# Kernel tuning notes

Hardware: AMD Instinct MI355X
Metric: run time of the kernel (lower is better)

Reference implementation:

```python
import jax, jax.numpy as jnp
import numpy as np

RATE, KEEP_K = 4, 1
TAU, ALPHA = 0.1, 0.7
LN_EPS = 1e-5


def setup_inputs() -> dict:
    key = jax.random.key(0)
    k1, k2, k3 = jax.random.split(key, 3)
    B, D, T = 16, 1024, 4096
    x = jax.random.normal(k1, (B, D, T), dtype=jnp.float32)
    W_proj = jax.random.normal(k2, (D, D), dtype=jnp.float32) * 0.02
    b_proj = jnp.zeros((D,), dtype=jnp.float32)
    ln_g = jnp.ones((D,), dtype=jnp.float32)
    ln_b = jnp.zeros((D,), dtype=jnp.float32)
    w_score = jax.random.normal(k3, (D,), dtype=jnp.float32) * 0.02
    return {"x": x, "W_proj": W_proj, "b_proj": b_proj,
            "ln_g": ln_g, "ln_b": ln_b, "w_score": w_score}


def reference(x, W_proj, b_proj, ln_g, ln_b, w_score):
    # x: [B, D, T]; chunks of width w=RATE along T (T divisible by RATE)
    B, D, T = x.shape
    C, w, k = T // RATE, RATE, KEEP_K
    r = w - k
    tokens = x.reshape(B, D, C, w).transpose(0, 2, 3, 1)          # [B,C,w,D]

    # metric_proj (torch Linear: y = x W^T + b), computed once and reused
    feat = jnp.einsum('bcwd,ed->bcwe', tokens, W_proj) + b_proj   # [B,C,w,D]

    # F.normalize(feat, dim=-1) with eps=1e-12
    nrm = jnp.maximum(jnp.linalg.norm(feat, axis=-1, keepdims=True), 1e-12)
    metric = feat / nrm
    sim = jnp.einsum('bcwd,bcvd->bcwv', metric, metric)           # [B,C,w,w]
    sim = jnp.where(jnp.eye(w, dtype=bool), 0.0, sim)

    # score head: LayerNorm(feat) @ w_score (no bias)
    mu = feat.mean(-1, keepdims=True)
    var = ((feat - mu) ** 2).mean(-1, keepdims=True)
    s_pred = jnp.einsum('bcwd,d->bcw',
                        ((feat - mu) / jnp.sqrt(var + LN_EPS)) * ln_g + ln_b,
                        w_score)                                   # [B,C,w]

    imp_norm = jnp.linalg.norm(tokens, axis=-1)                    # [B,C,w]
    s_mix = ALPHA * s_pred + (1.0 - ALPHA) * imp_norm
    attn = jax.nn.softmax(sim / TAU, axis=-1)                      # [B,C,w,w]

    # top-k kept tokens per chunk (descending, matches torch.topk)
    _, top_idx = jax.lax.top_k(s_mix, k)                           # [B,C,k]
    kept = jnp.take_along_axis(tokens, top_idx[..., None], axis=2) # [B,C,k,D]

    # rest indices: complement of top_idx in ascending order (matches nonzero)
    pos = jnp.arange(w)
    is_top = (pos[None, None, :, None] == top_idx[:, :, None, :]).any(-1)  # [B,C,w]
    keys = jnp.where(is_top, w, pos)
    rest_idx = jnp.argsort(keys, axis=-1)[..., :r]                 # [B,C,r]

    rest_tokens = jnp.take_along_axis(tokens, rest_idx[..., None], axis=2)  # [B,C,r,D]
    attn_rest = jnp.take_along_axis(attn, rest_idx[..., None], axis=2)      # [B,C,r,w]
    rest_imp = jnp.take_along_axis(attn_rest, top_idx[:, :, None, :], axis=3)  # [B,C,r,k]
    norm_w = rest_imp / (rest_imp.sum(-1, keepdims=True) + 1e-6)
    merged_add = jnp.einsum('bcrk,bcrd->bckd', norm_w, rest_tokens)  # [B,C,k,D]
    kept = kept + merged_add / 2.0

    out = kept.reshape(B, C * k, D).transpose(0, 2, 1)             # [B,D,C*k]
    return out
```

## Files before the change

### kernel.cpp

```cpp
#include <hip/hip_runtime.h>
#include <hip/hip_bf16.h>
#include <math.h>
#include <stdint.h>

#define D_DIM 1024
#define T_DIM 4096
#define B_DIM 16
#define C_DIM 1024
#define NCHUNK (B_DIM * C_DIM)
#define NKT 32
#define TPAIR (T_DIM/2)
#define EPAIR (D_DIM/2)
#define TAU_INV 10.0f
#define ALPHA 0.7f
#define LN_EPS 1e-5f
#define XSCALE 4.0f
#define WSCALE 32.0f
#define INV_SCALE (1.0f/128.0f)

typedef _Float16 h8 __attribute__((ext_vector_type(8)));
typedef float f4 __attribute__((ext_vector_type(4)));

static __device__ __forceinline__ void gload16(const void* g, void* s) {
    __builtin_amdgcn_global_load_lds(
        (const __attribute__((address_space(1))) unsigned int*)g,
        (__attribute__((address_space(3))) unsigned int*)s, 16, 0, 0);
}

__global__ __launch_bounds__(256)
void split_x_kernel(const float* __restrict__ x, uint4* __restrict__ Xh,
                    uint4* __restrict__ Xl)
{
    const int tid = threadIdx.x;
    const int t1 = blockIdx.x * 256;
    const int kt = blockIdx.y;
    const int b  = blockIdx.z;
    const int d0 = kt * 32;
    __shared__ __align__(16) float xs[32][264];
    const float* X = x + ((size_t)b * D_DIM + d0) * T_DIM + t1;
    #pragma unroll
    for (int i = 0; i < 8; i++) {
        int idx = tid + i * 256;
        int d = idx >> 6, tq = idx & 63;
        *(float4*)&xs[d][tq * 4] = *(const float4*)(X + (size_t)d * T_DIM + tq * 4);
    }
    __syncthreads();
    const size_t rowbase = (size_t)(b * NKT + kt) * TPAIR + (t1 >> 1);
    #pragma unroll
    for (int ch = 0; ch < 4; ch++) {
        int tp_l = ch * 32 + (tid >> 3);
        int sg = tid & 7;
        int pg = sg ^ (tp_l & 7);
        int p = pg >> 2, g = pg & 3;
        int tl = tp_l * 2 + p;
        unsigned hb[8], lb[8];
        #pragma unroll
        for (int j = 0; j < 8; j++) {
            float v = xs[g * 8 + j][tl] * XSCALE;
            _Float16 hv = (_Float16)v;
            float hf = (float)hv;
            _Float16 lv = (_Float16)(v - hf);
            hb[j] = (unsigned)__builtin_bit_cast(unsigned short, hv);
            lb[j] = (unsigned)__builtin_bit_cast(unsigned short, lv);
        }
        uint4 uh, ul;
        uh.x = hb[0] | (hb[1] << 16); uh.y = hb[2] | (hb[3] << 16);
        uh.z = hb[4] | (hb[5] << 16); uh.w = hb[6] | (hb[7] << 16);
        ul.x = lb[0] | (lb[1] << 16); ul.y = lb[2] | (lb[3] << 16);
        ul.z = lb[4] | (lb[5] << 16); ul.w = lb[6] | (lb[7] << 16);
        size_t si = (rowbase + tp_l) * 8 + sg;
        Xh[si] = uh; Xl[si] = ul;
    }
}

__global__ __launch_bounds__(256)
void split_w_kernel(const float* __restrict__ W, uint4* __restrict__ Wh,
                    uint4* __restrict__ Wl)
{
    const int tid = threadIdx.x;
    const int e1 = blockIdx.x * 256;
    const int kt = blockIdx.y;
    const int d0 = kt * 32;
    const size_t rowbase = (size_t)kt * EPAIR + (e1 >> 1);
    #pragma unroll
    for (int ch = 0; ch < 4; ch++) {
        int ep_l = ch * 32 + (tid >> 3);
        int sg = tid & 7;
        int pg = sg ^ (ep_l & 7);
        int p = pg >> 2, g = pg & 3;
        int e = e1 + ep_l * 2 + p;
        const float* src = W + (size_t)e * D_DIM + d0 + g * 8;
        float4 a = *(const float4*)src;
        float4 c = *(const float4*)(src + 4);
        float vv[8] = {a.x, a.y, a.z, a.w, c.x, c.y, c.z, c.w};
        unsigned hb[8], lb[8];
        #pragma unroll
        for (int j = 0; j < 8; j++) {
            float v = vv[j] * WSCALE;
            _Float16 hv = (_Float16)v;
            float hf = (float)hv;
            _Float16 lv = (_Float16)(v - hf);
            hb[j] = (unsigned)__builtin_bit_cast(unsigned short, hv);
            lb[j] = (unsigned)__builtin_bit_cast(unsigned short, lv);
        }
        uint4 uh, ul;
        uh.x = hb[0] | (hb[1] << 16); uh.y = hb[2] | (hb[3] << 16);
        uh.z = hb[4] | (hb[5] << 16); uh.w = hb[6] | (hb[7] << 16);
        ul.x = lb[0] | (lb[1] << 16); ul.y = lb[2] | (lb[3] << 16);
        ul.z = lb[4] | (lb[5] << 16); ul.w = lb[6] | (lb[7] << 16);
        size_t si = (rowbase + ep_l) * 8 + sg;
        Wh[si] = uh; Wl[si] = ul;
    }
}

__global__ __launch_bounds__(256, 2)
void gemm_mfma_kernel(const uint4* __restrict__ Xh, const uint4* __restrict__ Xl,
                      const uint4* __restrict__ Wh, const uint4* __restrict__ Wl,
                      const float* __restrict__ b_proj, const float* __restrict__ ln_g,
                      const float* __restrict__ w_score, float* __restrict__ scal)
{
    const int tid = threadIdx.x;
    const int l   = tid & 63;
    const int wid = tid >> 6;
    const int wm  = wid >> 1, we = wid & 1;

    int sid = blockIdx.x;
    int xcd = sid & 7, jj = sid >> 3;
    int panel = xcd * 64 + (jj >> 3);
    int eblk  = jj & 7;
    int b = panel >> 5, tblk = panel & 31;
    const int t0 = tblk * 128, e0 = eblk * 128;

    __shared__ __align__(16) char lds[32768];
    char* sXh = lds;
    char* sXl = lds + 8192;
    char* sWh = lds + 16384;
    char* sWl = lds + 24576;

    const int h    = (l & 15) >> 1;
    const int slot = (((l & 1) << 2) | (l >> 4)) ^ h;
    const int aoff = (wm * 32 + h) * 128 + slot * 16;
    const int boff = (we * 32 + h) * 128 + slot * 16;

    f4 acc[4][4];
    #pragma unroll
    for (int mi = 0; mi < 4; mi++)
        #pragma unroll
        for (int ni = 0; ni < 4; ni++) acc[mi][ni] = (f4){0.f, 0.f, 0.f, 0.f};

    const char* gXh0 = (const char*)Xh + ((size_t)b * NKT * TPAIR + (size_t)(t0 >> 1)) * 128;
    const char* gXl0 = (const char*)Xl + ((size_t)b * NKT * TPAIR + (size_t)(t0 >> 1)) * 128;
    const char* gWh0 = (const char*)Wh + (size_t)(e0 >> 1) * 128;
    const char* gWl0 = (const char*)Wl + (size_t)(e0 >> 1) * 128;

    const int stg = wid * 2048;
    const int lo16 = l * 16;

    for (int kt = 0; kt < NKT; kt++) {
        const char* pxh = gXh0 + (size_t)kt * (TPAIR * 128);
        const char* pxl = gXl0 + (size_t)kt * (TPAIR * 128);
        const char* pwh = gWh0 + (size_t)kt * (EPAIR * 128);
        const char* pwl = gWl0 + (size_t)kt * (EPAIR * 128);
        gload16(pxh + stg + lo16,        sXh + stg);
        gload16(pxh + stg + 1024 + lo16, sXh + stg + 1024);
        gload16(pxl + stg + lo16,        sXl + stg);
        gload16(pxl + stg + 1024 + lo16, sXl + stg + 1024);
        gload16(pwh + stg + lo16,        sWh + stg);
        gload16(pwh + stg + 1024 + lo16, sWh + stg + 1024);
        gload16(pwl + stg + lo16,        sWl + stg);
        gload16(pwl + stg + 1024 + lo16, sWl + stg + 1024);
        __syncthreads();

        h8 ah[4], al[4], bh[4], bl[4];
        #pragma unroll
        for (int mi = 0; mi < 4; mi++) {
            ah[mi] = *(const h8*)(sXh + aoff + mi * 1024);
            al[mi] = *(const h8*)(sXl + aoff + mi * 1024);
        }
        #pragma unroll
        for (int ni = 0; ni < 4; ni++) {
            bh[ni] = *(const h8*)(sWh + boff + ni * 1024);
            bl[ni] = *(const h8*)(sWl + boff + ni * 1024);
        }
        #pragma unroll
        for (int mi = 0; mi < 4; mi++)
            #pragma unroll
            for (int ni = 0; ni < 4; ni++) {
                acc[mi][ni] = __builtin_amdgcn_mfma_f32_16x16x32_f16(ah[mi], bh[ni], acc[mi][ni], 0, 0, 0);
                acc[mi][ni] = __builtin_amdgcn_mfma_f32_16x16x32_f16(ah[mi], bl[ni], acc[mi][ni], 0, 0, 0);
                acc[mi][ni] = __builtin_amdgcn_mfma_f32_16x16x32_f16(al[mi], bh[ni], acc[mi][ni], 0, 0, 0);
            }
        __syncthreads();
    }

    const int ecol = l & 15;
    float bias[4], q1[4];
    #pragma unroll
    for (int ni = 0; ni < 4; ni++) {
        int e = e0 + we * 64 + ni * 16 + ecol;
        bias[ni] = b_proj[e];
        q1[ni]   = ln_g[e] * w_score[e];
    }
    #pragma unroll
    for (int mi = 0; mi < 4; mi++) {
        float f[4][4];
        #pragma unroll
        for (int ni = 0; ni < 4; ni++)
            #pragma unroll
            for (int r = 0; r < 4; r++)
                f[r][ni] = acc[mi][ni][r] * INV_SCALE + bias[ni];
        float red[18];
        int pi = 0;
        #pragma unroll
        for (int a2 = 0; a2 < 4; a2++)
            #pragma unroll
            for (int b2 = a2; b2 < 4; b2++) {
                float s = 0.f;
                #pragma unroll
                for (int ni = 0; ni < 4; ni++) s = fmaf(f[a2][ni], f[b2][ni], s);
                red[pi++] = s;
            }
        #pragma unroll
        for (int a2 = 0; a2 < 4; a2++) {
            float s1 = 0.f, s2 = 0.f;
            #pragma unroll
            for (int ni = 0; ni < 4; ni++) {
                s1 = fmaf(f[a2][ni], q1[ni], s1);
                s2 += f[a2][ni];
            }
            red[10 + a2] = s1;
            red[14 + a2] = s2;
        }
        #pragma unroll
        for (int v = 0; v < 18; v++) {
            float s = red[v];
            s += __shfl_xor(s, 1);
            s += __shfl_xor(s, 2);
            s += __shfl_xor(s, 4);
            s += __shfl_xor(s, 8);
            red[v] = s;
        }
        if ((l & 15) == 0) {
            int chunk = b * C_DIM + (t0 >> 2) + wm * 16 + mi * 4 + (l >> 4);
            float* dst = scal + (size_t)chunk * 18;
            #pragma unroll
            for (int v = 0; v < 18; v++) atomicAdd(dst + v, red[v]);
        }
    }
}

__global__ __launch_bounds__(256, 2)
void gemm_reduce_kernel(const float* __restrict__ x, const float* __restrict__ W,
                        const float* __restrict__ b_proj, const float* __restrict__ ln_g,
                        const float* __restrict__ w_score, float* __restrict__ scal)
{
    const int tid = threadIdx.x;
    const int tx  = tid & 15;
    const int ty  = tid >> 4;
    const int t0  = blockIdx.x * 128;
    const int e0  = blockIdx.y * 128;
    const int b   = blockIdx.z;
    const float* X = x + (size_t)b * D_DIM * T_DIM;

    __shared__ __align__(16) float Xs[32][128];
    __shared__ __align__(16) float Ws[32][132];

    float acc[8][8];
    #pragma unroll
    for (int i = 0; i < 8; i++)
        #pragma unroll
        for (int j = 0; j < 8; j++) acc[i][j] = 0.f;

    for (int k0 = 0; k0 < D_DIM; k0 += 32) {
        #pragma unroll
        for (int i = 0; i < 4; i++) {
            int idx = tid + i * 256;
            int dr = idx >> 5, cl = idx & 31;
            const float4 v = *(const float4*)(X + (size_t)(k0 + dr) * T_DIM + t0 + cl * 4);
            *(float4*)&Xs[dr][cl * 4] = v;
        }
        #pragma unroll
        for (int i = 0; i < 4; i++) {
            int idx = tid + i * 256;
            int er = idx >> 3, ck = idx & 7;
            const float4 v = *(const float4*)(W + (size_t)(e0 + er) * D_DIM + k0 + ck * 4);
            Ws[ck * 4 + 0][er] = v.x;
            Ws[ck * 4 + 1][er] = v.y;
            Ws[ck * 4 + 2][er] = v.z;
            Ws[ck * 4 + 3][er] = v.w;
        }
        __syncthreads();
        #pragma unroll 8
        for (int k = 0; k < 32; k++) {
            const float4 xa = *(const float4*)&Xs[k][ty * 8];
            const float4 xb = *(const float4*)&Xs[k][ty * 8 + 4];
            const float4 wa = *(const float4*)&Ws[k][tx * 4];
            const float4 wb = *(const float4*)&Ws[k][64 + tx * 4];
            const float xm[8] = {xa.x, xa.y, xa.z, xa.w, xb.x, xb.y, xb.z, xb.w};
            const float wn[8] = {wa.x, wa.y, wa.z, wa.w, wb.x, wb.y, wb.z, wb.w};
            #pragma unroll
            for (int i = 0; i < 8; i++)
                #pragma unroll
                for (int j = 0; j < 8; j++)
                    acc[i][j] = fmaf(xm[i], wn[j], acc[i][j]);
        }
        __syncthreads();
    }

    float bv[8], q1v[8];
    #pragma unroll
    for (int j = 0; j < 8; j++) {
        int n = (j < 4) ? (tx * 4 + j) : (64 + tx * 4 + (j - 4));
        int e = e0 + n;
        bv[j]  = b_proj[e];
        q1v[j] = ln_g[e] * w_score[e];
    }
    #pragma unroll
    for (int i = 0; i < 8; i++)
        #pragma unroll
        for (int j = 0; j < 8; j++) acc[i][j] += bv[j];

    #pragma unroll
    for (int hh = 0; hh < 2; hh++) {
        float red[18];
        int p = 0;
        #pragma unroll
        for (int a = 0; a < 4; a++)
            #pragma unroll
            for (int b2 = a; b2 < 4; b2++) {
                float s = 0.f;
                #pragma unroll
                for (int j = 0; j < 8; j++) s = fmaf(acc[hh * 4 + a][j], acc[hh * 4 + b2][j], s);
                red[p++] = s;
            }
        #pragma unroll
        for (int a = 0; a < 4; a++) {
            float s1 = 0.f, s2 = 0.f;
            #pragma unroll
            for (int j = 0; j < 8; j++) {
                s1 = fmaf(acc[hh * 4 + a][j], q1v[j], s1);
                s2 += acc[hh * 4 + a][j];
            }
            red[10 + a] = s1;
            red[14 + a] = s2;
        }
        #pragma unroll
        for (int v = 0; v < 18; v++) {
            float s = red[v];
            s += __shfl_xor(s, 1);
            s += __shfl_xor(s, 2);
            s += __shfl_xor(s, 4);
            s += __shfl_xor(s, 8);
            red[v] = s;
        }
        if (tx == 0) {
            int chunk = b * C_DIM + (t0 >> 2) + ty * 2 + hh;
            float* dst = scal + (size_t)chunk * 18;
            #pragma unroll
            for (int v = 0; v < 18; v++) atomicAdd(dst + v, red[v]);
        }
    }
}

__global__ __launch_bounds__(256, 4)
void toknorm_kernel(const float* __restrict__ x, float* __restrict__ tokN2)
{
    const int tt = threadIdx.x & 63;
    const int ds = threadIdx.x >> 6;
    const int t  = blockIdx.x * 64 + tt;
    const int b  = blockIdx.y;
    const float* X = x + (size_t)b * D_DIM * T_DIM + t;
    float s = 0.f;
    const int d0 = ds * 256;
    for (int d = d0; d < d0 + 256; d++) {
        float v = X[(size_t)d * T_DIM];
        s = fmaf(v, v, s);
    }
    __shared__ float lred[256];
    lred[threadIdx.x] = s;
    __syncthreads();
    if (ds == 0)
        tokN2[b * T_DIM + t] = lred[tt] + lred[64 + tt] + lred[128 + tt] + lred[192 + tt];
}

__global__ __launch_bounds__(256, 4)
void coef_kernel(const float* __restrict__ scal, const float* __restrict__ tokN2,
                 const float* __restrict__ ln_g, const float* __restrict__ ln_b,
                 const float* __restrict__ w_score, float* __restrict__ coef)
{
    const int tid = threadIdx.x;
    float p1 = 0.f, p2 = 0.f;
    for (int d = tid; d < D_DIM; d += 256) {
        float wsv = w_score[d];
        p1 = fmaf(ln_g[d], wsv, p1);
        p2 = fmaf(ln_b[d], wsv, p2);
    }
    __shared__ float r1[256], r2[256];
    r1[tid] = p1; r2[tid] = p2;
    __syncthreads();
    for (int s = 128; s > 0; s >>= 1) {
        if (tid < s) { r1[tid] += r1[tid + s]; r2[tid] += r2[tid + s]; }
        __syncthreads();
    }
    const float c1 = r1[0], c2 = r2[0];

    const int chunk = blockIdx.x * 256 + tid;
    const float* s = scal + (size_t)chunk * 18;
    float G[4][4];
    G[0][0] = s[0]; G[0][1] = s[1]; G[0][2] = s[2]; G[0][3] = s[3];
    G[1][1] = s[4]; G[1][2] = s[5]; G[1][3] = s[6];
    G[2][2] = s[7]; G[2][3] = s[8]; G[3][3] = s[9];
    G[1][0] = G[0][1]; G[2][0] = G[0][2]; G[3][0] = G[0][3];
    G[2][1] = G[1][2]; G[3][1] = G[1][3]; G[3][2] = G[2][3];

    const int b = chunk >> 10;
    const int c = chunk & 1023;

    float smix[4], nrm[4];
    #pragma unroll
    for (int i = 0; i < 4; i++) {
        float mu  = s[14 + i] * (1.f / 1024.f);
        float var = G[i][i] * (1.f / 1024.f) - mu * mu;
        float sig = sqrtf(var + LN_EPS);
        float spred = (s[10 + i] - mu * c1) / sig + c2;
        float imp = sqrtf(tokN2[b * T_DIM + c * 4 + i]);
        smix[i] = ALPHA * spred + (1.f - ALPHA) * imp;
        nrm[i]  = fmaxf(sqrtf(G[i][i]), 1e-12f);
    }
    int top = 0; float best = smix[0];
    #pragma unroll
    for (int i = 1; i < 4; i++)
        if (smix[i] > best) { best = smix[i]; top = i; }

    float sim[4][4];
    #pragma unroll
    for (int i = 0; i < 4; i++)
        #pragma unroll
        for (int j = 0; j < 4; j++)
            sim[i][j] = (i == j) ? 0.f : G[i][j] / (nrm[i] * nrm[j]);

    float cf[4];
    #pragma unroll
    for (int r = 0; r < 4; r++) {
        if (r == top) { cf[r] = 1.f; continue; }
        float z[4], m = -1e30f;
        #pragma unroll
        for (int j = 0; j < 4; j++) { z[j] = sim[r][j] * TAU_INV; m = fmaxf(m, z[j]); }
        float denom = 0.f, num = 0.f;
        #pragma unroll
        for (int j = 0; j < 4; j++) {
            float e = expf(z[j] - m);
            denom += e;
            if (j == top) num = e;
        }
        float a = num / denom;
        cf[r] = 0.5f * (a / (a + 1e-6f));
    }
    *(float4*)(coef + (size_t)chunk * 4) = make_float4(cf[0], cf[1], cf[2], cf[3]);
}

__global__ __launch_bounds__(256, 8)
void out_kernel(const float* __restrict__ x, const float* __restrict__ coef,
                float* __restrict__ out)
{
    const size_t gid = (size_t)blockIdx.x * 256 + threadIdx.x;
    const int    c   = (int)(gid & 1023);
    const size_t bd  = gid >> 10;
    const int    b   = (int)(bd >> 10);
    const float4 xv = *(const float4*)(x + (bd << 12) + (size_t)c * 4);
    const float4 cf = *(const float4*)(coef + ((size_t)(b << 10) + c) * 4);
    out[gid] = xv.x * cf.x + xv.y * cf.y + xv.z * cf.z + xv.w * cf.w;
}

extern "C" void kernel_launch(void* const* d_in, const int* in_sizes, int n_in,
                              void* d_out, int out_size, void* d_ws, size_t ws_size,
                              hipStream_t stream)
{
    const float* x   = (const float*)d_in[0];
    const float* W   = (const float*)d_in[1];
    const float* bp  = (const float*)d_in[2];
    const float* g   = (const float*)d_in[3];
    const float* lb  = (const float*)d_in[4];
    const float* wsc = (const float*)d_in[5];
    float* out = (float*)d_out;

    const size_t XH_BYTES = (size_t)B_DIM * NKT * TPAIR * 128;
    const size_t WH_BYTES = (size_t)NKT * EPAIR * 128;
    const size_t NEED = 2 * XH_BYTES + 2 * WH_BYTES
                      + (size_t)NCHUNK * 18 * 4 + (size_t)B_DIM * T_DIM * 4
                      + (size_t)NCHUNK * 4 * 4;

    if (ws_size >= NEED) {
        char* w0 = (char*)d_ws;
        uint4* Xh = (uint4*)w0;
        uint4* Xl = (uint4*)(w0 + XH_BYTES);
        uint4* Wh = (uint4*)(w0 + 2 * XH_BYTES);
        uint4* Wl = (uint4*)(w0 + 2 * XH_BYTES + WH_BYTES);
        float* scal  = (float*)(w0 + 2 * XH_BYTES + 2 * WH_BYTES);
        float* tokN2 = scal + (size_t)NCHUNK * 18;
        float* coef  = tokN2 + (size_t)B_DIM * T_DIM;

        hipMemsetAsync(scal, 0, (size_t)NCHUNK * 18 * sizeof(float), stream);
        split_x_kernel<<<dim3(T_DIM / 256, NKT, B_DIM), 256, 0, stream>>>(x, Xh, Xl);
        split_w_kernel<<<dim3(D_DIM / 256, NKT), 256, 0, stream>>>(W, Wh, Wl);
        toknorm_kernel<<<dim3(T_DIM / 64, B_DIM), 256, 0, stream>>>(x, tokN2);
        gemm_mfma_kernel<<<4096, 256, 0, stream>>>(Xh, Xl, Wh, Wl, bp, g, wsc, scal);
        coef_kernel<<<NCHUNK / 256, 256, 0, stream>>>(scal, tokN2, g, lb, wsc, coef);
        out_kernel<<<(B_DIM * D_DIM * C_DIM) / 256, 256, 0, stream>>>(x, coef, out);
    } else {
        float* scal  = (float*)d_ws;
        float* tokN2 = scal + (size_t)NCHUNK * 18;
        float* coef  = tokN2 + (size_t)B_DIM * T_DIM;

        hipMemsetAsync(scal, 0, (size_t)NCHUNK * 18 * sizeof(float), stream);
        dim3 gA(T_DIM / 128, D_DIM / 128, B_DIM);
        gemm_reduce_kernel<<<gA, 256, 0, stream>>>(x, W, bp, g, wsc, scal);
        toknorm_kernel<<<dim3(T_DIM / 64, B_DIM), 256, 0, stream>>>(x, tokN2);
        coef_kernel<<<NCHUNK / 256, 256, 0, stream>>>(scal, tokN2, g, lb, wsc, coef);
        out_kernel<<<(B_DIM * D_DIM * C_DIM) / 256, 256, 0, stream>>>(x, coef, out);
    }
}
```

Before: 1.326 ms.

## Double-buffer GEMM LDS tiles and fuse token-norm into split_x

The MFMA GEMM main loop now uses two 32KB LDS buffers: it prefetches the next k-tile via global_load_lds while computing on the current one, which halves the barriers per iteration and hides load latency. The token squared-norm computation is folded into split_x_kernel using atomicAdd per token, removing the separate toknorm kernel and its extra full read of x. The cost is doubled LDS (64KB), which may limit occupancy against the 2-blocks-per-CU launch bound, plus atomic traffic on tokN2.

```diff
diff --git a/kernel.cpp b/kernel.cpp
--- a/kernel.cpp
+++ b/kernel.cpp
@@ -29,7 +29,7 @@
 
 __global__ __launch_bounds__(256)
 void split_x_kernel(const float* __restrict__ x, uint4* __restrict__ Xh,
-                    uint4* __restrict__ Xl)
+                    uint4* __restrict__ Xl, float* __restrict__ tokN2)
 {
     const int tid = threadIdx.x;
     const int t1 = blockIdx.x * 256;
@@ -54,9 +54,12 @@
         int p = pg >> 2, g = pg & 3;
         int tl = tp_l * 2 + p;
         unsigned hb[8], lb[8];
+        float n2 = 0.f;
         #pragma unroll
         for (int j = 0; j < 8; j++) {
-            float v = xs[g * 8 + j][tl] * XSCALE;
+            float raw = xs[g * 8 + j][tl];
+            n2 = fmaf(raw, raw, n2);
+            float v = raw * XSCALE;
             _Float16 hv = (_Float16)v;
             float hf = (float)hv;
             _Float16 lv = (_Float16)(v - hf);
@@ -70,6 +73,7 @@
         ul.z = lb[4] | (lb[5] << 16); ul.w = lb[6] | (lb[7] << 16);
         size_t si = (rowbase + tp_l) * 8 + sg;
         Xh[si] = uh; Xl[si] = ul;
+        atomicAdd(&tokN2[b * T_DIM + t1 + tl], n2);
     }
 }
 
@@ -131,11 +135,7 @@
     int b = panel >> 5, tblk = panel & 31;
     const int t0 = tblk * 128, e0 = eblk * 128;
 
-    __shared__ __align__(16) char lds[32768];
-    char* sXh = lds;
-    char* sXl = lds + 8192;
-    char* sWh = lds + 16384;
-    char* sWl = lds + 24576;
+    __shared__ __align__(16) char lds[65536];
 
     const int h    = (l & 15) >> 1;
     const int slot = (((l & 1) << 2) | (l >> 4)) ^ h;
@@ -156,31 +156,33 @@
     const int stg = wid * 2048;
     const int lo16 = l * 16;
 
-    for (int kt = 0; kt < NKT; kt++) {
+    auto stage = [&](int off, int kt) {
         const char* pxh = gXh0 + (size_t)kt * (TPAIR * 128);
         const char* pxl = gXl0 + (size_t)kt * (TPAIR * 128);
         const char* pwh = gWh0 + (size_t)kt * (EPAIR * 128);
         const char* pwl = gWl0 + (size_t)kt * (EPAIR * 128);
-        gload16(pxh + stg + lo16,        sXh + stg);
-        gload16(pxh + stg + 1024 + lo16, sXh + stg + 1024);
-        gload16(pxl + stg + lo16,        sXl + stg);
-        gload16(pxl + stg + 1024 + lo16, sXl + stg + 1024);
-        gload16(pwh + stg + lo16,        sWh + stg);
-        gload16(pwh + stg + 1024 + lo16, sWh + stg + 1024);
-        gload16(pwl + stg + lo16,        sWl + stg);
-        gload16(pwl + stg + 1024 + lo16, sWl + stg + 1024);
-        __syncthreads();
-
+        char* base = lds + off;
+        gload16(pxh + stg + lo16,        base + stg);
+        gload16(pxh + stg + 1024 + lo16, base + stg + 1024);
+        gload16(pxl + stg + lo16,        base + 8192 + stg);
+        gload16(pxl + stg + 1024 + lo16, base + 8192 + stg + 1024);
+        gload16(pwh + stg + lo16,        base + 16384 + stg);
+        gload16(pwh + stg + 1024 + lo16, base + 16384 + stg + 1024);
+        gload16(pwl + stg + lo16,        base + 24576 + stg);
+        gload16(pwl + stg + 1024 + lo16, base + 24576 + stg + 1024);
+    };
+    auto compute = [&](int off) {
+        const char* base = lds + off;
         h8 ah[4], al[4], bh[4], bl[4];
         #pragma unroll
         for (int mi = 0; mi < 4; mi++) {
-            ah[mi] = *(const h8*)(sXh + aoff + mi * 1024);
-            al[mi] = *(const h8*)(sXl + aoff + mi * 1024);
+            ah[mi] = *(const h8*)(base + aoff + mi * 1024);
+            al[mi] = *(const h8*)(base + 8192 + aoff + mi * 1024);
         }
         #pragma unroll
         for (int ni = 0; ni < 4; ni++) {
-            bh[ni] = *(const h8*)(sWh + boff + ni * 1024);
-            bl[ni] = *(const h8*)(sWl + boff + ni * 1024);
+            bh[ni] = *(const h8*)(base + 16384 + boff + ni * 1024);
+            bl[ni] = *(const h8*)(base + 24576 + boff + ni * 1024);
         }
         #pragma unroll
         for (int mi = 0; mi < 4; mi++)
@@ -190,8 +192,22 @@
                 acc[mi][ni] = __builtin_amdgcn_mfma_f32_16x16x32_f16(ah[mi], bl[ni], acc[mi][ni], 0, 0, 0);
                 acc[mi][ni] = __builtin_amdgcn_mfma_f32_16x16x32_f16(al[mi], bh[ni], acc[mi][ni], 0, 0, 0);
             }
-        __syncthreads();
-    }
+    };
+
+    stage(0, 0);
+    asm volatile("s_waitcnt vmcnt(0)" ::: "memory");
+    __builtin_amdgcn_s_barrier();
+
+    int off = 0;
+    #pragma unroll 1
+    for (int kt = 0; kt < NKT - 1; kt++) {
+        stage(off ^ 32768, kt + 1);
+        compute(off);
+        asm volatile("s_waitcnt vmcnt(0)" ::: "memory");
+        __builtin_amdgcn_s_barrier();
+        off ^= 32768;
+    }
+    compute(off);
 
     const int ecol = l & 15;
     float bias[4], q1[4];
@@ -500,10 +516,11 @@
         float* tokN2 = scal + (size_t)NCHUNK * 18;
         float* coef  = tokN2 + (size_t)B_DIM * T_DIM;
 
-        hipMemsetAsync(scal, 0, (size_t)NCHUNK * 18 * sizeof(float), stream);
-        split_x_kernel<<<dim3(T_DIM / 256, NKT, B_DIM), 256, 0, stream>>>(x, Xh, Xl);
+        hipMemsetAsync(scal, 0,
+                       ((size_t)NCHUNK * 18 + (size_t)B_DIM * T_DIM) * sizeof(float),
+                       stream);
+        split_x_kernel<<<dim3(T_DIM / 256, NKT, B_DIM), 256, 0, stream>>>(x, Xh, Xl, tokN2);
         split_w_kernel<<<dim3(D_DIM / 256, NKT), 256, 0, stream>>>(W, Wh, Wl);
-        toknorm_kernel<<<dim3(T_DIM / 64, B_DIM), 256, 0, stream>>>(x, tokN2);
         gemm_mfma_kernel<<<4096, 256, 0, stream>>>(Xh, Xl, Wh, Wl, bp, g, wsc, scal);
         coef_kernel<<<NCHUNK / 256, 256, 0, stream>>>(scal, tokN2, g, lb, wsc, coef);
         out_kernel<<<(B_DIM * D_DIM * C_DIM) / 256, 256, 0, stream>>>(x, coef, out);
```

New measurement: 1.781 ms. 1.34x slower.

## Enlarge MFMA GEMM tile to 256x256 with double-buffered LDS pipeline

Applied to the files above, without the earlier changes.

The split-fp16 GEMM now uses 512-thread blocks computing 256x256 tiles (8x4 accumulators per wave) with a 128KB double-buffered LDS. Global-to-LDS loads for the next k-step are issued in four phases interleaved with MFMA work, using explicit waitcnt, barriers and setprio in place of the previous load-sync-compute-sync loop. The aim is to raise data reuse per loaded byte and hide global load latency behind matrix math. In exchange it adds register pressure from 128 accumulator floats plus fragments, and the large LDS allocation limits how many blocks fit per CU.

```diff
diff --git a/kernel.cpp b/kernel.cpp
--- a/kernel.cpp
+++ b/kernel.cpp
@@ -27,6 +27,11 @@
         (__attribute__((address_space(3))) unsigned int*)s, 16, 0, 0);
 }
 
+#define VMCNT0 asm volatile("s_waitcnt vmcnt(0)" ::: "memory")
+#define LGKM0  asm volatile("s_waitcnt lgkmcnt(0)" ::: "memory")
+#define BAR    __builtin_amdgcn_s_barrier()
+#define SCHEDB __builtin_amdgcn_sched_barrier(0)
+
 __global__ __launch_bounds__(256)
 void split_x_kernel(const float* __restrict__ x, uint4* __restrict__ Xh,
                     uint4* __restrict__ Xl)
@@ -113,7 +118,7 @@
     }
 }
 
-__global__ __launch_bounds__(256, 2)
+__global__ __launch_bounds__(512, 2)
 void gemm_mfma_kernel(const uint4* __restrict__ Xh, const uint4* __restrict__ Xl,
                       const uint4* __restrict__ Wh, const uint4* __restrict__ Wl,
                       const float* __restrict__ b_proj, const float* __restrict__ ln_g,
@@ -122,29 +127,26 @@
     const int tid = threadIdx.x;
     const int l   = tid & 63;
     const int wid = tid >> 6;
-    const int wm  = wid >> 1, we = wid & 1;
-
-    int sid = blockIdx.x;
-    int xcd = sid & 7, jj = sid >> 3;
-    int panel = xcd * 64 + (jj >> 3);
-    int eblk  = jj & 7;
-    int b = panel >> 5, tblk = panel & 31;
-    const int t0 = tblk * 128, e0 = eblk * 128;
-
-    __shared__ __align__(16) char lds[32768];
-    char* sXh = lds;
-    char* sXl = lds + 8192;
-    char* sWh = lds + 16384;
-    char* sWl = lds + 24576;
+    const int wm  = wid >> 2;
+    const int we  = wid & 3;
+
+    int sid  = blockIdx.x;
+    int xcd  = sid & 7, jj = sid >> 3;
+    int eblk = jj & 3;
+    int panel = xcd * 32 + (jj >> 2);
+    int b = panel >> 4, tblk = panel & 15;
+    const int t0 = tblk * 256, e0 = eblk * 256;
+
+    __shared__ __align__(16) char lds[131072];
 
     const int h    = (l & 15) >> 1;
     const int slot = (((l & 1) << 2) | (l >> 4)) ^ h;
-    const int aoff = (wm * 32 + h) * 128 + slot * 16;
-    const int boff = (we * 32 + h) * 128 + slot * 16;
-
-    f4 acc[4][4];
-    #pragma unroll
-    for (int mi = 0; mi < 4; mi++)
+    const int abase = (wm * 64 + h) * 128 + slot * 16;
+    const int bbase = (we * 32 + h) * 128 + slot * 16;
+
+    f4 acc[8][4];
+    #pragma unroll
+    for (int mi = 0; mi < 8; mi++)
         #pragma unroll
         for (int ni = 0; ni < 4; ni++) acc[mi][ni] = (f4){0.f, 0.f, 0.f, 0.f};
 
@@ -153,44 +155,79 @@
     const char* gWh0 = (const char*)Wh + (size_t)(e0 >> 1) * 128;
     const char* gWl0 = (const char*)Wl + (size_t)(e0 >> 1) * 128;
 
-    const int stg = wid * 2048;
-    const int lo16 = l * 16;
-
+    const int sw = wid * 2048;
+    const int lo = l * 16;
+
+    auto stage1 = [&](const char* src, char* dstbase) {
+        gload16(src + sw + lo,        dstbase + sw);
+        gload16(src + sw + 1024 + lo, dstbase + sw + 1024);
+    };
+    auto trip = [&](const h8& ah_, const h8& al_, const h8& bh_, const h8& bl_, f4& c) {
+        c = __builtin_amdgcn_mfma_f32_16x16x32_f16(ah_, bh_, c, 0, 0, 0);
+        c = __builtin_amdgcn_mfma_f32_16x16x32_f16(ah_, bl_, c, 0, 0, 0);
+        c = __builtin_amdgcn_mfma_f32_16x16x32_f16(al_, bh_, c, 0, 0, 0);
+    };
+
+    {
+        stage1(gXh0, lds);
+        stage1(gXl0, lds + 16384);
+        stage1(gWh0, lds + 32768);
+        stage1(gWl0, lds + 49152);
+    }
+
+    h8 bh0, bh1, bh2, bh3, bl0, bl1, bl2, bl3;
+    int off = 0;
+    #pragma unroll 1
     for (int kt = 0; kt < NKT; kt++) {
-        const char* pxh = gXh0 + (size_t)kt * (TPAIR * 128);
-        const char* pxl = gXl0 + (size_t)kt * (TPAIR * 128);
-        const char* pwh = gWh0 + (size_t)kt * (EPAIR * 128);
-        const char* pwl = gWl0 + (size_t)kt * (EPAIR * 128);
-        gload16(pxh + stg + lo16,        sXh + stg);
-        gload16(pxh + stg + 1024 + lo16, sXh + stg + 1024);
-        gload16(pxl + stg + lo16,        sXl + stg);
-        gload16(pxl + stg + 1024 + lo16, sXl + stg + 1024);
-        gload16(pwh + stg + lo16,        sWh + stg);
-        gload16(pwh + stg + 1024 + lo16, sWh + stg + 1024);
-        gload16(pwl + stg + lo16,        sWl + stg);
-        gload16(pwl + stg + 1024 + lo16, sWl + stg + 1024);
-        __syncthreads();
-
-        h8 ah[4], al[4], bh[4], bl[4];
-        #pragma unroll
-        for (int mi = 0; mi < 4; mi++) {
-            ah[mi] = *(const h8*)(sXh + aoff + mi * 1024);
-            al[mi] = *(const h8*)(sXl + aoff + mi * 1024);
-        }
-        #pragma unroll
-        for (int ni = 0; ni < 4; ni++) {
-            bh[ni] = *(const h8*)(sWh + boff + ni * 1024);
-            bl[ni] = *(const h8*)(sWl + boff + ni * 1024);
-        }
-        #pragma unroll
-        for (int mi = 0; mi < 4; mi++)
-            #pragma unroll
-            for (int ni = 0; ni < 4; ni++) {
-                acc[mi][ni] = __builtin_amdgcn_mfma_f32_16x16x32_f16(ah[mi], bh[ni], acc[mi][ni], 0, 0, 0);
-                acc[mi][ni] = __builtin_amdgcn_mfma_f32_16x16x32_f16(ah[mi], bl[ni], acc[mi][ni], 0, 0, 0);
-                acc[mi][ni] = __builtin_amdgcn_mfma_f32_16x16x32_f16(al[mi], bh[ni], acc[mi][ni], 0, 0, 0);
-            }
-        __syncthreads();
+        VMCNT0;
+        BAR;
+        const char* cb = lds + off;
+        char* nb = lds + (off ^ 65536);
+        const bool st = (kt + 1 < NKT);
+        const size_t k1 = (size_t)(kt + 1);
+        const char* pxh = gXh0 + k1 * (TPAIR * 128);
+        const char* pxl = gXl0 + k1 * (TPAIR * 128);
+        const char* pwh = gWh0 + k1 * (EPAIR * 128);
+        const char* pwl = gWl0 + k1 * (EPAIR * 128);
+
+#define PHASE(p, SRC, DSTOFF)                                                   \
+        {                                                                       \
+            h8 a0h = *(const h8*)(cb + abase + (p) * 2048);                     \
+            h8 a0l = *(const h8*)(cb + 16384 + abase + (p) * 2048);             \
+            h8 a1h = *(const h8*)(cb + abase + (p) * 2048 + 1024);              \
+            h8 a1l = *(const h8*)(cb + 16384 + abase + (p) * 2048 + 1024);      \
+            if ((p) == 0) {                                                     \
+                bh0 = *(const h8*)(cb + 32768 + bbase);                         \
+                bh1 = *(const h8*)(cb + 32768 + bbase + 1024);                  \
+                bh2 = *(const h8*)(cb + 32768 + bbase + 2048);                  \
+                bh3 = *(const h8*)(cb + 32768 + bbase + 3072);                  \
+                bl0 = *(const h8*)(cb + 49152 + bbase);                         \
+                bl1 = *(const h8*)(cb + 49152 + bbase + 1024);                  \
+                bl2 = *(const h8*)(cb + 49152 + bbase + 2048);                  \
+                bl3 = *(const h8*)(cb + 49152 + bbase + 3072);                  \
+            }                                                                   \
+            if (st) stage1(SRC, nb + DSTOFF);                                   \
+            BAR;                                                                \
+            LGKM0; SCHEDB;                                                      \
+            __builtin_amdgcn_s_setprio(1);                                      \
+            trip(a0h, a0l, bh0, bl0, acc[2*(p)][0]);                            \
+            trip(a0h, a0l, bh1, bl1, acc[2*(p)][1]);                            \
+            trip(a0h, a0l, bh2, bl2, acc[2*(p)][2]);                            \
+            trip(a0h, a0l, bh3, bl3, acc[2*(p)][3]);                            \
+            trip(a1h, a1l, bh0, bl0, acc[2*(p)+1][0]);                          \
+            trip(a1h, a1l, bh1, bl1, acc[2*(p)+1][1]);                          \
+            trip(a1h, a1l, bh2, bl2, acc[2*(p)+1][2]);                          \
+            trip(a1h, a1l, bh3, bl3, acc[2*(p)+1][3]);                          \
+            __builtin_amdgcn_s_setprio(0);                                      \
+            BAR;                                                                \
+        }
+
+        PHASE(0, pxh, 0)
+        PHASE(1, pxl, 16384)
+        PHASE(2, pwh, 32768)
+        PHASE(3, pwl, 49152)
+#undef PHASE
+        off ^= 65536;
     }
 
     const int ecol = l & 15;
@@ -202,7 +239,7 @@
         q1[ni]   = ln_g[e] * w_score[e];
     }
     #pragma unroll
-    for (int mi = 0; mi < 4; mi++) {
+    for (int mi = 0; mi < 8; mi++) {
         float f[4][4];
         #pragma unroll
         for (int ni = 0; ni < 4; ni++)
@@ -241,7 +278,7 @@
             red[v] = s;
         }
         if ((l & 15) == 0) {
-            int chunk = b * C_DIM + (t0 >> 2) + wm * 16 + mi * 4 + (l >> 4);
+            int chunk = b * C_DIM + ((t0 + wm * 128 + mi * 16) >> 2) + (l >> 4);
             float* dst = scal + (size_t)chunk * 18;
             #pragma unroll
             for (int v = 0; v < 18; v++) atomicAdd(dst + v, red[v]);
@@ -504,7 +541,7 @@
         split_x_kernel<<<dim3(T_DIM / 256, NKT, B_DIM), 256, 0, stream>>>(x, Xh, Xl);
         split_w_kernel<<<dim3(D_DIM / 256, NKT), 256, 0, stream>>>(W, Wh, Wl);
         toknorm_kernel<<<dim3(T_DIM / 64, B_DIM), 256, 0, stream>>>(x, tokN2);
-        gemm_mfma_kernel<<<4096, 256, 0, stream>>>(Xh, Xl, Wh, Wl, bp, g, wsc, scal);
+        gemm_mfma_kernel<<<1024, 512, 0, stream>>>(Xh, Xl, Wh, Wl, bp, g, wsc, scal);
         coef_kernel<<<NCHUNK / 256, 256, 0, stream>>>(scal, tokN2, g, lb, wsc, coef);
         out_kernel<<<(B_DIM * D_DIM * C_DIM) / 256, 256, 0, stream>>>(x, coef, out);
     } else {
```

Measured after the change: 1.318 ms. Within noise of the previous version (-0.6%).
